# Optimization experiments

Measured on AMD Instinct MI355X. Metric: run time of the kernel, lower is better.

Reference implementation:

```python
import jax, jax.numpy as jnp
import numpy as np

GROUPS = 8
EPS = 1e-5
V, CIN, COUT, K, TDIM, B = 49152, 128, 256, 8, 256, 1
E = V * 9


def group_norm(x, gamma, beta):
    # x: [B, V, C]; torch GroupNorm semantics: normalize over (pixels, channels-in-group)
    b, v, c = x.shape
    xg = x.reshape(b, v, GROUPS, c // GROUPS)
    mu = xg.mean(axis=(1, 3), keepdims=True)
    var = xg.var(axis=(1, 3), keepdims=True)
    xg = (xg - mu) * jax.lax.rsqrt(var + EPS)
    return xg.reshape(b, v, c) * gamma + beta


def cheb_conv(x, row, col, vals, w):
    # x: [B, V, C]; w: [K, C, F]; Chebyshev recurrence on sparse Laplacian
    b, v, c = x.shape
    k = w.shape[0]
    xt = x.transpose(1, 0, 2).reshape(v, b * c)  # [V, B*C]

    def spmv(z):  # sparse L @ z via scatter-add
        return jnp.zeros_like(z).at[row].add(vals[:, None] * z[col])

    terms = [xt]
    if k > 1:
        terms.append(spmv(xt))
    for _ in range(k - 2):
        terms.append(2.0 * spmv(terms[-1]) - terms[-2])
    t = jnp.stack(terms).reshape(k, v, b, c)  # [K, V, B, C]
    return jnp.einsum('kvbc,kcf->bvf', t, w)  # [B, V, F]


def setup_inputs() -> dict:
    key = jax.random.key(0)
    ks = jax.random.split(key, 12)
    return {
        'x': jax.random.normal(ks[0], (B, V, CIN), jnp.float32),
        'time_emb': jax.random.normal(ks[1], (B, TDIM), jnp.float32),
        'row': jax.random.randint(ks[2], (E,), 0, V),
        'col': jax.random.randint(ks[3], (E,), 0, V),
        'vals': jax.random.normal(ks[4], (E,), jnp.float32) * 0.1,
        'w_res': jax.random.normal(ks[5], (K, CIN, COUT), jnp.float32) * 0.05,
        'w1': jax.random.normal(ks[6], (K, CIN, COUT), jnp.float32) * 0.05,
        'w2': jax.random.normal(ks[7], (K, COUT, COUT), jnp.float32) * 0.05,
        'g1': jnp.ones((CIN,), jnp.float32),
        'b1': jnp.zeros((CIN,), jnp.float32),
        'g2': jnp.ones((COUT,), jnp.float32),
        'b2': jnp.zeros((COUT,), jnp.float32),
        'wt': jax.random.normal(ks[8], (TDIM, COUT), jnp.float32) * 0.05,
        'bt': jnp.zeros((COUT,), jnp.float32),
    }


def reference(x, time_emb, row, col, vals, w_res, w1, w2, g1, b1, g2, b2, wt, bt):
    # conv_res (in_channels != out_channels), pooling = identity
    res = cheb_conv(x, row, col, vals, w_res)
    # block1: conv(silu(group_norm(x)))
    h = cheb_conv(jax.nn.silu(group_norm(x, g1, b1)), row, col, vals, w1)
    # time embedding: SiLU -> Linear -> broadcast over pixels
    h = h + (jax.nn.silu(time_emb) @ wt + bt)[:, None, :]
    # block2
    h = cheb_conv(jax.nn.silu(group_norm(h, g2, b2)), row, col, vals, w2)
    return h + res
```

## Files before the change

kernel.cpp:

```cpp
#include <hip/hip_runtime.h>
#include <cstddef>

#define V_N 49152
#define E_N 442368
#define GEPS 1e-5f
#define CO 256
#define TD 256

typedef _Float16 h16;
typedef _Float16 h8v __attribute__((ext_vector_type(8)));
typedef _Float16 h4v __attribute__((ext_vector_type(4)));
typedef float f4v __attribute__((ext_vector_type(4)));

__device__ __forceinline__ void gload_lds16(const void* g, void* l) {
    __builtin_amdgcn_global_load_lds(
        (const __attribute__((address_space(1))) unsigned int*)g,
        (__attribute__((address_space(3))) unsigned int*)l, 16, 0, 0);
}

__global__ void count_edges(const int* __restrict__ row, int* __restrict__ cnt) {
    int e = blockIdx.x * blockDim.x + threadIdx.x;
    if (e < E_N) atomicAdd(&cnt[row[e]], 1);
}

__global__ void scan_rowptr(int* __restrict__ cnt, int* __restrict__ rowptr) {
    __shared__ int part[1024];
    const int CHUNK = V_N / 1024;
    int t = threadIdx.x;
    int base = t * CHUNK;
    int s = 0;
    for (int i = 0; i < CHUNK; ++i) s += cnt[base + i];
    part[t] = s;
    __syncthreads();
    for (int off = 1; off < 1024; off <<= 1) {
        int v = part[t];
        int add = (t >= off) ? part[t - off] : 0;
        __syncthreads();
        part[t] = v + add;
        __syncthreads();
    }
    int run = (t == 0) ? 0 : part[t - 1];
    for (int i = 0; i < CHUNK; ++i) {
        int c = cnt[base + i];
        rowptr[base + i] = run;
        cnt[base + i] = run;
        run += c;
    }
    if (t == 1023) rowptr[V_N] = run;
}

__global__ void fill_csr(const int* __restrict__ row, const int* __restrict__ col,
                         const float* __restrict__ vals, int* __restrict__ cursor,
                         int2* __restrict__ ep) {
    int e = blockIdx.x * blockDim.x + threadIdx.x;
    if (e < E_N) {
        int r = row[e];
        int slot = atomicAdd(&cursor[r], 1);
        ep[slot] = make_int2(col[e], __float_as_int(vals[e]));
    }
}

__global__ void wprep(const float* __restrict__ w, h16* __restrict__ wt, int KC) {
    __shared__ float t[16][17];
    int kc = blockIdx.x * 16 + threadIdx.y;
    int f = blockIdx.y * 16 + threadIdx.x;
    t[threadIdx.y][threadIdx.x] = w[(size_t)kc * CO + f];
    __syncthreads();
    int fo = blockIdx.y * 16 + threadIdx.y;
    int kco = blockIdx.x * 16 + threadIdx.x;
    wt[(size_t)fo * KC + kco] = (h16)t[threadIdx.x][threadIdx.y];
}

template <int C>
__global__ void gn_stats2(const float* __restrict__ x, const float* __restrict__ tvec,
                          float* __restrict__ part) {
    __shared__ float ls[8], lss[8];
    int t = threadIdx.x;
    if (t < 8) { ls[t] = 0.f; lss[t] = 0.f; }
    __syncthreads();
    const int total4 = V_N * (C / 4);
    const int cmask = (C / 4) - 1;
    const int stride = gridDim.x * blockDim.x;
    int i0 = blockIdx.x * blockDim.x + t;
    const int c4 = i0 & cmask;
    float t0 = 0.f, t1 = 0.f, t2 = 0.f, t3 = 0.f;
    if (tvec) {
        t0 = tvec[c4 * 4 + 0]; t1 = tvec[c4 * 4 + 1];
        t2 = tvec[c4 * 4 + 2]; t3 = tvec[c4 * 4 + 3];
    }
    float s = 0.f, ss = 0.f;
    for (int i = i0; i < total4; i += stride) {
        float4 v = ((const float4*)x)[i];
        v.x += t0; v.y += t1; v.z += t2; v.w += t3;
        s  += v.x + v.y + v.z + v.w;
        ss += v.x * v.x + v.y * v.y + v.z * v.z + v.w * v.w;
    }
    constexpr int GL = (C == 128) ? 4 : 8;
#pragma unroll
    for (int off = 1; off < GL; off <<= 1) {
        s  += __shfl_xor(s, off);
        ss += __shfl_xor(ss, off);
    }
    int lane = t & 63;
    if ((lane & (GL - 1)) == 0) {
        int g = c4 >> ((C == 128) ? 2 : 3);
        atomicAdd(&ls[g], s);
        atomicAdd(&lss[g], ss);
    }
    __syncthreads();
    if (t < 16) part[blockIdx.x * 16 + t] = (t < 8) ? ls[t] : lss[t - 8];
}

#define GN_BLOCKS 512

__global__ void gn_reduce(const float* __restrict__ part, float* __restrict__ stats,
                          int nb) {
    __shared__ float acc[16];
    int t = threadIdx.x;
    if (t < 16) acc[t] = 0.f;
    __syncthreads();
    int idx = t & 15;
    float s = 0.f;
    for (int j = t >> 4; j < nb; j += 16) s += part[j * 16 + idx];
    atomicAdd(&acc[idx], s);
    __syncthreads();
    if (t < 16) stats[t] = acc[t];
}

__global__ void gn1_apply(const float* __restrict__ x, const float* __restrict__ stats,
                          const float* __restrict__ gamma, const float* __restrict__ beta,
                          h16* __restrict__ dst, int ldT) {
    const float Ng = (float)V_N * 16.f;
    const int total4 = V_N * 32;
    for (int i = blockIdx.x * blockDim.x + threadIdx.x; i < total4;
         i += gridDim.x * blockDim.x) {
        int c4 = i & 31;
        int v = i >> 5;
        float4 xv = ((const float4*)x)[i];
        float in[4] = {xv.x, xv.y, xv.z, xv.w};
        h4v o, oc;
#pragma unroll
        for (int j = 0; j < 4; ++j) {
            int c = c4 * 4 + j;
            int g = c >> 4;
            float mu = stats[g] / Ng;
            float var = stats[8 + g] / Ng - mu * mu;
            float rs = rsqrtf(var + GEPS);
            float y = (in[j] - mu) * rs * gamma[c] + beta[c];
            y = y / (1.f + expf(-y));
            o[j] = (h16)y;
            oc[j] = (h16)in[j];
        }
        size_t base = (size_t)v * ldT + c4 * 4;
        *(h4v*)&dst[base] = o;
        *(h4v*)&dst[base + 128] = oc;
    }
}

__global__ void gn2_apply(const float* __restrict__ x, const float* __restrict__ tvec,
                          const float* __restrict__ stats, const float* __restrict__ gamma,
                          const float* __restrict__ beta, h16* __restrict__ dst, int ldT) {
    const float Ng = (float)V_N * 32.f;
    const int total4 = V_N * 64;
    for (int i = blockIdx.x * blockDim.x + threadIdx.x; i < total4;
         i += gridDim.x * blockDim.x) {
        int c4 = i & 63;
        int v = i >> 6;
        float4 xv = ((const float4*)x)[i];
        float in[4] = {xv.x, xv.y, xv.z, xv.w};
        h4v o;
#pragma unroll
        for (int j = 0; j < 4; ++j) {
            int c = c4 * 4 + j;
            int g = c >> 5;
            float mu = stats[g] / Ng;
            float var = stats[8 + g] / Ng - mu * mu;
            float rs = rsqrtf(var + GEPS);
            float val = in[j] + tvec[c];
            float y = (val - mu) * rs * gamma[c] + beta[c];
            y = y / (1.f + expf(-y));
            o[j] = (h16)y;
        }
        *(h4v*)&dst[(size_t)v * ldT + c4 * 4] = o;
    }
}

__global__ void time_mlp(const float* __restrict__ te, const float* __restrict__ wt,
                         const float* __restrict__ bt, float* __restrict__ tvec) {
    __shared__ float s[TD];
    int f = threadIdx.x;
    float v = te[f];
    s[f] = v / (1.f + expf(-v));
    __syncthreads();
    float acc = bt[f];
    for (int t = 0; t < TD; ++t) acc += s[t] * wt[t * CO + f];
    tvec[f] = acc;
}

template <bool RECUR>
__global__ void spmv2(const int* __restrict__ rowptr, const int2* __restrict__ ep,
                      const h16* __restrict__ zb, const h16* __restrict__ pb,
                      h16* __restrict__ db, int ldT) {
    int wid = threadIdx.x >> 6, lane = threadIdx.x & 63;
    int v = blockIdx.x * 4 + wid;
    int s = rowptr[v], e = rowptr[v + 1];
    int half = lane >> 5, hl = lane & 31;
    float acc[8];
#pragma unroll
    for (int i = 0; i < 8; ++i) acc[i] = 0.f;
    for (int j = s; j < e; j += 2) {
        int jj = j + half;
        int jm = (jj < e) ? jj : (e - 1);
        int2 p = ep[jm];
        float val = (jj < e) ? __int_as_float(p.y) : 0.f;
        h8v z = *(const h8v*)&zb[(size_t)p.x * ldT + hl * 8];
#pragma unroll
        for (int i = 0; i < 8; ++i) acc[i] += val * (float)z[i];
    }
#pragma unroll
    for (int i = 0; i < 8; ++i) acc[i] += __shfl_xor(acc[i], 32);
    if (half == 0) {
        size_t base = (size_t)v * ldT + hl * 8;
        h8v o;
        if (RECUR) {
            h8v pv = *(const h8v*)&pb[base];
#pragma unroll
            for (int i = 0; i < 8; ++i) o[i] = (h16)(2.f * acc[i] - (float)pv[i]);
        } else {
#pragma unroll
            for (int i = 0; i < 8; ++i) o[i] = (h16)acc[i];
        }
        *(h8v*)&db[base] = o;
    }
}

template <bool ACC>
__global__ __launch_bounds__(256, 2) void gemm_f16(const h16* __restrict__ A, int lda,
                                                   const h16* __restrict__ Wt, int ldw,
                                                   int wofs, int KC, int ksh,
                                                   float* __restrict__ out) {
    __shared__ h16 As[128 * 32];
    __shared__ h16 Bs[256 * 32];
    const int tid = threadIdx.x;
    const int wid = tid >> 6, lane = tid & 63;
    const int m0 = blockIdx.x * 128;
    const int wm = wid & 1, wn = wid >> 1;
    const int fr = lane & 15, fq = lane >> 4;
    const int rl = lane >> 2;
    const int qs = (lane & 3) ^ ((lane >> 3) & 3);
    const int kmsk = (1 << ksh) - 1;
    const h16* Wb = Wt + wofs;

    f4v acc[4][8];
#pragma unroll
    for (int i = 0; i < 4; ++i)
#pragma unroll
        for (int n = 0; n < 8; ++n) acc[i][n] = (f4v){0.f, 0.f, 0.f, 0.f};

    for (int k0 = 0; k0 < KC; k0 += 32) {
        int ca = (((k0 >> ksh) << 8) | (k0 & kmsk)) + qs * 8;
        int cb = k0 + qs * 8;
        __syncthreads();
#pragma unroll
        for (int j = 0; j < 2; ++j) {
            int rbase = wid * 32 + j * 16;
            gload_lds16(A + (size_t)(m0 + rbase + rl) * lda + ca, &As[rbase * 32]);
        }
#pragma unroll
        for (int j = 0; j < 4; ++j) {
            int rbase = wid * 64 + j * 16;
            gload_lds16(Wb + (size_t)(rbase + rl) * ldw + cb, &Bs[rbase * 32]);
        }
        __syncthreads();
        const int slot = (fq ^ ((fr >> 1) & 3)) * 8;
        h8v af[4], bf[8];
#pragma unroll
        for (int i = 0; i < 4; ++i)
            af[i] = *(const h8v*)&As[(wm * 64 + i * 16 + fr) * 32 + slot];
#pragma unroll
        for (int n = 0; n < 8; ++n)
            bf[n] = *(const h8v*)&Bs[(wn * 128 + n * 16 + fr) * 32 + slot];
#pragma unroll
        for (int i = 0; i < 4; ++i)
#pragma unroll
            for (int n = 0; n < 8; ++n)
                acc[i][n] = __builtin_amdgcn_mfma_f32_16x16x32_f16(af[i], bf[n],
                                                                   acc[i][n], 0, 0, 0);
    }
#pragma unroll
    for (int i = 0; i < 4; ++i)
#pragma unroll
        for (int n = 0; n < 8; ++n)
#pragma unroll
            for (int rr = 0; rr < 4; ++rr) {
                int row = m0 + wm * 64 + i * 16 + fq * 4 + rr;
                int col = wn * 128 + n * 16 + fr;
                size_t idx = (size_t)row * CO + col;
                if (ACC) out[idx] += acc[i][n][rr];
                else out[idx] = acc[i][n][rr];
            }
}

static void launch_gemm(hipStream_t s, bool acc, const h16* A, int lda, const h16* Wt,
                        int ldw, int wofs, int KC, int ksh, float* out) {
    dim3 g(V_N / 128);
    if (acc) gemm_f16<true><<<g, 256, 0, s>>>(A, lda, Wt, ldw, wofs, KC, ksh, out);
    else     gemm_f16<false><<<g, 256, 0, s>>>(A, lda, Wt, ldw, wofs, KC, ksh, out);
}

static void chain_spmv(hipStream_t s, int chunk, int k0, int kend, h16* terms, int ldT,
                       const int* rp, const int2* ep) {
    for (int k = (k0 == 0 ? 1 : k0); k < kend; ++k) {
        const h16* zb = terms + ((k - 1) % chunk) * 256;
        h16* db = terms + (k % chunk) * 256;
        if (k == 1) {
            spmv2<false><<<V_N / 4, 256, 0, s>>>(rp, ep, zb, nullptr, db, ldT);
        } else {
            const h16* pb = terms + ((k - 2) % chunk) * 256;
            spmv2<true><<<V_N / 4, 256, 0, s>>>(rp, ep, zb, pb, db, ldT);
        }
    }
}

extern "C" void kernel_launch(void* const* d_in, const int* in_sizes, int n_in,
                              void* d_out, int out_size, void* d_ws, size_t ws_size,
                              hipStream_t stream) {
    const float* x    = (const float*)d_in[0];
    const float* te   = (const float*)d_in[1];
    const int*   row  = (const int*)d_in[2];
    const int*   col  = (const int*)d_in[3];
    const float* vals = (const float*)d_in[4];
    const float* wres = (const float*)d_in[5];
    const float* w1   = (const float*)d_in[6];
    const float* w2   = (const float*)d_in[7];
    const float* g1   = (const float*)d_in[8];
    const float* b1   = (const float*)d_in[9];
    const float* g2   = (const float*)d_in[10];
    const float* b2   = (const float*)d_in[11];
    const float* wt   = (const float*)d_in[12];
    const float* bt   = (const float*)d_in[13];
    float* out = (float*)d_out;

    const size_t slot_b = (size_t)V_N * 256 * 2;
    const size_t res_b  = (size_t)V_N * 256 * 4;
    const size_t csr_b  = (size_t)(V_N + V_N + 1) * 4 + (size_t)E_N * 8;
    const size_t wt_b   = (size_t)(1024 + 2048 + 1024) * CO * 2;
    const size_t misc_b = 8192 + (size_t)GN_BLOCKS * 16 * 4;
    auto need = [&](int ch) { return (size_t)ch * slot_b + res_b + csr_b + wt_b + misc_b; };
    int chunk = (ws_size >= need(8)) ? 8 : (ws_size >= need(4)) ? 4 : 2;
    if (ws_size < need(2)) return;
    const int ldT = chunk * 256;

    char* p = (char*)d_ws;
    h16* terms = (h16*)p;              p += (size_t)chunk * slot_b;
    float* resbuf = (float*)p;         p += res_b;
    h16* w1t = (h16*)p;                p += (size_t)1024 * CO * 2;
    h16* w2t = (h16*)p;                p += (size_t)2048 * CO * 2;
    h16* wrt = (h16*)p;                p += (size_t)1024 * CO * 2;
    int* cnt = (int*)p;                p += (size_t)V_N * 4;
    int* rp  = (int*)p;                p += (size_t)(V_N + 1) * 4;
    int2* ep = (int2*)p;               p += (size_t)E_N * 8;
    float* stats = (float*)p;          p += 64;
    float* tv = (float*)p;             p += 1024;
    float* gpart = (float*)p;          p += (size_t)GN_BLOCKS * 16 * 4;

    hipMemsetAsync(cnt, 0, V_N * sizeof(int), stream);
    count_edges<<<E_N / 256, 256, 0, stream>>>(row, cnt);
    scan_rowptr<<<1, 1024, 0, stream>>>(cnt, rp);
    fill_csr<<<E_N / 256, 256, 0, stream>>>(row, col, vals, cnt, ep);

    wprep<<<dim3(1024 / 16, 16), dim3(16, 16), 0, stream>>>(w1, w1t, 1024);
    wprep<<<dim3(2048 / 16, 16), dim3(16, 16), 0, stream>>>(w2, w2t, 2048);
    wprep<<<dim3(1024 / 16, 16), dim3(16, 16), 0, stream>>>(wres, wrt, 1024);

    time_mlp<<<1, 256, 0, stream>>>(te, wt, bt, tv);

    gn_stats2<128><<<GN_BLOCKS, 256, 0, stream>>>(x, nullptr, gpart);
    gn_reduce<<<1, 256, 0, stream>>>(gpart, stats, GN_BLOCKS);
    gn1_apply<<<2048, 256, 0, stream>>>(x, stats, g1, b1, terms, ldT);

    for (int k0 = 0; k0 < 8; k0 += chunk) {
        int kend = (k0 + chunk < 8) ? k0 + chunk : 8;
        chain_spmv(stream, chunk, k0, kend, terms, ldT, rp, ep);
        int KC = (kend - k0) * 128;
        bool acc = (k0 > 0);
        launch_gemm(stream, acc, terms,       ldT, w1t, 1024, k0 * 128, KC, 7, out);
        launch_gemm(stream, acc, terms + 128, ldT, wrt, 1024, k0 * 128, KC, 7, resbuf);
    }

    gn_stats2<256><<<GN_BLOCKS, 256, 0, stream>>>(out, tv, gpart);
    gn_reduce<<<1, 256, 0, stream>>>(gpart, stats, GN_BLOCKS);
    gn2_apply<<<2048, 256, 0, stream>>>(out, tv, stats, g2, b2, terms, ldT);

    hipMemcpyAsync(out, resbuf, res_b, hipMemcpyDeviceToDevice, stream);

    for (int k0 = 0; k0 < 8; k0 += chunk) {
        int kend = (k0 + chunk < 8) ? k0 + chunk : 8;
        chain_spmv(stream, chunk, k0, kend, terms, ldT, rp, ep);
        int KC = (kend - k0) * 256;
        launch_gemm(stream, true, terms, ldT, w2t, 2048, k0 * 256, KC, 8, out);
    }
}
```

Measured before the change: 949.8 us.

## Shrink GEMM tile, merge dual GEMMs, fuse residual add, unroll SpMV edges

The GEMM drops from 128-row to 64-row tiles with three blocks per CU. The w1 and w_res GEMMs now run in one launch via a second grid dimension. The first block2 GEMM reads the residual buffer as its bias, which removes the device-to-device memcpy. The SpMV inner loop handles four edges per iteration so two gathers are in flight per lane, and the chunk size is capped at 4. The trade-offs are more K-chunk launches, read-modify-write accumulation passes over the fp32 output, and smaller tiles with less weight reuse per block.

Measured after the change: 882.7 us. 1.08x faster.

```diff
diff --git a/kernel.cpp b/kernel.cpp
--- a/kernel.cpp
+++ b/kernel.cpp
@@ -208,14 +208,18 @@
     float acc[8];
 #pragma unroll
     for (int i = 0; i < 8; ++i) acc[i] = 0.f;
-    for (int j = s; j < e; j += 2) {
-        int jj = j + half;
-        int jm = (jj < e) ? jj : (e - 1);
-        int2 p = ep[jm];
-        float val = (jj < e) ? __int_as_float(p.y) : 0.f;
-        h8v z = *(const h8v*)&zb[(size_t)p.x * ldT + hl * 8];
-#pragma unroll
-        for (int i = 0; i < 8; ++i) acc[i] += val * (float)z[i];
+    for (int j = s; j < e; j += 4) {
+        int j0 = j + half, j1 = j + half + 2;
+        int2 p0 = ep[(j0 < e) ? j0 : (e - 1)];
+        int2 p1 = ep[(j1 < e) ? j1 : (e - 1)];
+        float v0 = (j0 < e) ? __int_as_float(p0.y) : 0.f;
+        float v1 = (j1 < e) ? __int_as_float(p1.y) : 0.f;
+        h8v z0 = *(const h8v*)&zb[(size_t)p0.x * ldT + hl * 8];
+        h8v z1 = *(const h8v*)&zb[(size_t)p1.x * ldT + hl * 8];
+#pragma unroll
+        for (int i = 0; i < 8; ++i) acc[i] += v0 * (float)z0[i];
+#pragma unroll
+        for (int i = 0; i < 8; ++i) acc[i] += v1 * (float)z1[i];
     }
 #pragma unroll
     for (int i = 0; i < 8; ++i) acc[i] += __shfl_xor(acc[i], 32);
@@ -234,38 +238,35 @@
     }
 }
 
-template <bool ACC>
-__global__ __launch_bounds__(256, 2) void gemm_f16(const h16* __restrict__ A, int lda,
-                                                   const h16* __restrict__ Wt, int ldw,
-                                                   int wofs, int KC, int ksh,
-                                                   float* __restrict__ out) {
-    __shared__ h16 As[128 * 32];
+template <int MODE, bool DUAL>
+__global__ __launch_bounds__(256, 3) void gemm_f16(
+    const h16* __restrict__ A, int lda, const h16* __restrict__ Wt,
+    const h16* __restrict__ Wt2, int ldw, int wofs, int KC, int ksh,
+    const float* __restrict__ bias, float* __restrict__ out,
+    float* __restrict__ out2) {
+    __shared__ h16 As[64 * 32];
     __shared__ h16 Bs[256 * 32];
+    if (DUAL && blockIdx.y) { A += 128; Wt = Wt2; out = out2; }
     const int tid = threadIdx.x;
     const int wid = tid >> 6, lane = tid & 63;
-    const int m0 = blockIdx.x * 128;
-    const int wm = wid & 1, wn = wid >> 1;
+    const int m0 = blockIdx.x * 64;
     const int fr = lane & 15, fq = lane >> 4;
     const int rl = lane >> 2;
     const int qs = (lane & 3) ^ ((lane >> 3) & 3);
     const int kmsk = (1 << ksh) - 1;
     const h16* Wb = Wt + wofs;
 
-    f4v acc[4][8];
+    f4v acc[4][4];
 #pragma unroll
     for (int i = 0; i < 4; ++i)
 #pragma unroll
-        for (int n = 0; n < 8; ++n) acc[i][n] = (f4v){0.f, 0.f, 0.f, 0.f};
+        for (int n = 0; n < 4; ++n) acc[i][n] = (f4v){0.f, 0.f, 0.f, 0.f};
 
     for (int k0 = 0; k0 < KC; k0 += 32) {
         int ca = (((k0 >> ksh) << 8) | (k0 & kmsk)) + qs * 8;
         int cb = k0 + qs * 8;
         __syncthreads();
-#pragma unroll
-        for (int j = 0; j < 2; ++j) {
-            int rbase = wid * 32 + j * 16;
-            gload_lds16(A + (size_t)(m0 + rbase + rl) * lda + ca, &As[rbase * 32]);
-        }
+        gload_lds16(A + (size_t)(m0 + wid * 16 + rl) * lda + ca, &As[(wid * 16) * 32]);
 #pragma unroll
         for (int j = 0; j < 4; ++j) {
             int rbase = wid * 64 + j * 16;
@@ -273,39 +274,33 @@
         }
         __syncthreads();
         const int slot = (fq ^ ((fr >> 1) & 3)) * 8;
-        h8v af[4], bf[8];
+        h8v af[4], bf[4];
 #pragma unroll
         for (int i = 0; i < 4; ++i)
-            af[i] = *(const h8v*)&As[(wm * 64 + i * 16 + fr) * 32 + slot];
-#pragma unroll
-        for (int n = 0; n < 8; ++n)
-            bf[n] = *(const h8v*)&Bs[(wn * 128 + n * 16 + fr) * 32 + slot];
+            af[i] = *(const h8v*)&As[(i * 16 + fr) * 32 + slot];
+#pragma unroll
+        for (int n = 0; n < 4; ++n)
+            bf[n] = *(const h8v*)&Bs[(wid * 64 + n * 16 + fr) * 32 + slot];
 #pragma unroll
         for (int i = 0; i < 4; ++i)
 #pragma unroll
-            for (int n = 0; n < 8; ++n)
+            for (int n = 0; n < 4; ++n)
                 acc[i][n] = __builtin_amdgcn_mfma_f32_16x16x32_f16(af[i], bf[n],
                                                                    acc[i][n], 0, 0, 0);
     }
 #pragma unroll
     for (int i = 0; i < 4; ++i)
 #pragma unroll
-        for (int n = 0; n < 8; ++n)
+        for (int n = 0; n < 4; ++n)
 #pragma unroll
             for (int rr = 0; rr < 4; ++rr) {
-                int row = m0 + wm * 64 + i * 16 + fq * 4 + rr;
-                int col = wn * 128 + n * 16 + fr;
+                int row = m0 + i * 16 + fq * 4 + rr;
+                int col = wid * 64 + n * 16 + fr;
                 size_t idx = (size_t)row * CO + col;
-                if (ACC) out[idx] += acc[i][n][rr];
-                else out[idx] = acc[i][n][rr];
+                if (MODE == 0) out[idx] = acc[i][n][rr];
+                else if (MODE == 1) out[idx] += acc[i][n][rr];
+                else out[idx] = bias[idx] + acc[i][n][rr];
             }
-}
-
-static void launch_gemm(hipStream_t s, bool acc, const h16* A, int lda, const h16* Wt,
-                        int ldw, int wofs, int KC, int ksh, float* out) {
-    dim3 g(V_N / 128);
-    if (acc) gemm_f16<true><<<g, 256, 0, s>>>(A, lda, Wt, ldw, wofs, KC, ksh, out);
-    else     gemm_f16<false><<<g, 256, 0, s>>>(A, lda, Wt, ldw, wofs, KC, ksh, out);
 }
 
 static void chain_spmv(hipStream_t s, int chunk, int k0, int kend, h16* terms, int ldT,
@@ -347,7 +342,7 @@
     const size_t wt_b   = (size_t)(1024 + 2048 + 1024) * CO * 2;
     const size_t misc_b = 8192 + (size_t)GN_BLOCKS * 16 * 4;
     auto need = [&](int ch) { return (size_t)ch * slot_b + res_b + csr_b + wt_b + misc_b; };
-    int chunk = (ws_size >= need(8)) ? 8 : (ws_size >= need(4)) ? 4 : 2;
+    int chunk = (ws_size >= need(4)) ? 4 : 2;
     if (ws_size < need(2)) return;
     const int ldT = chunk * 256;
 
@@ -383,21 +378,29 @@
         int kend = (k0 + chunk < 8) ? k0 + chunk : 8;
         chain_spmv(stream, chunk, k0, kend, terms, ldT, rp, ep);
         int KC = (kend - k0) * 128;
-        bool acc = (k0 > 0);
-        launch_gemm(stream, acc, terms,       ldT, w1t, 1024, k0 * 128, KC, 7, out);
-        launch_gemm(stream, acc, terms + 128, ldT, wrt, 1024, k0 * 128, KC, 7, resbuf);
+        dim3 g(V_N / 64, 2);
+        if (k0 == 0)
+            gemm_f16<0, true><<<g, 256, 0, stream>>>(terms, ldT, w1t, wrt, 1024,
+                                                     k0 * 128, KC, 7, nullptr, out, resbuf);
+        else
+            gemm_f16<1, true><<<g, 256, 0, stream>>>(terms, ldT, w1t, wrt, 1024,
+                                                     k0 * 128, KC, 7, nullptr, out, resbuf);
     }
 
     gn_stats2<256><<<GN_BLOCKS, 256, 0, stream>>>(out, tv, gpart);
     gn_reduce<<<1, 256, 0, stream>>>(gpart, stats, GN_BLOCKS);
     gn2_apply<<<2048, 256, 0, stream>>>(out, tv, stats, g2, b2, terms, ldT);
-
-    hipMemcpyAsync(out, resbuf, res_b, hipMemcpyDeviceToDevice, stream);
 
     for (int k0 = 0; k0 < 8; k0 += chunk) {
         int kend = (k0 + chunk < 8) ? k0 + chunk : 8;
         chain_spmv(stream, chunk, k0, kend, terms, ldT, rp, ep);
         int KC = (kend - k0) * 256;
-        launch_gemm(stream, true, terms, ldT, w2t, 2048, k0 * 256, KC, 8, out);
-    }
-}
+        dim3 g(V_N / 64);
+        if (k0 == 0)
+            gemm_f16<2, false><<<g, 256, 0, stream>>>(terms, ldT, w2t, nullptr, 2048,
+                                                      0, KC, 8, resbuf, out, nullptr);
+        else
+            gemm_f16<1, false><<<g, 256, 0, stream>>>(terms, ldT, w2t, nullptr, 2048,
+                                                      k0 * 256, KC, 8, nullptr, out, nullptr);
+    }
+}
```
